# Kernel tuning notes

Measured on AMD Instinct MI355X. Metric: run time of the kernel, lower is better.

## Reference

```python
import jax, jax.numpy as jnp
import numpy as np
from jax import lax

B, N, D, H, K = 4096, 25, 256, 8, 3  # batch*frames, nodes, d_model, heads, conv kernel


def _layernorm(x, g, b, eps=1e-5):
    mu = jnp.mean(x, axis=-1, keepdims=True)
    var = jnp.var(x, axis=-1, keepdims=True)
    return (x - mu) * lax.rsqrt(var + eps) * g + b


def _conv1d(x_bdn, w):
    # x_bdn: [B, D, N], w: [D_out, D_in, K], padding=K//2 (same as torch Conv1d)
    return lax.conv_general_dilated(x_bdn, w, window_strides=(1,),
                                    padding=[(K // 2, K // 2)],
                                    dimension_numbers=('NCH', 'OIH', 'NCH'))


def setup_inputs() -> dict:
    key = jax.random.key(0)
    ks = jax.random.split(key, 12)
    x = jax.random.normal(ks[0], (B, N, D), dtype=jnp.float32)
    # symmetric adjacency with self-loops (skeleton graph surrogate)
    a = jax.random.bernoulli(ks[1], 0.3, (N, N))
    adj = a | a.T | jnp.eye(N, dtype=bool)
    cs = 1.0 / np.sqrt(D * K)
    wq = jax.random.normal(ks[2], (D, D, K), dtype=jnp.float32) * cs
    wk = jax.random.normal(ks[3], (D, D, K), dtype=jnp.float32) * cs
    wv = jax.random.normal(ks[4], (D, D, K), dtype=jnp.float32) * cs
    gq = jnp.ones((D,), jnp.float32); bq = jnp.zeros((D,), jnp.float32)
    gk = jnp.ones((D,), jnp.float32); bk = jnp.zeros((D,), jnp.float32)
    gv = jnp.ones((D,), jnp.float32); bv = jnp.zeros((D,), jnp.float32)
    rel_table = jax.random.normal(ks[5], (2 * N - 1, H), dtype=jnp.float32) * 0.02
    local_bias = jnp.zeros((H, N, N), jnp.float32)
    wo = jax.random.normal(ks[6], (D, D), dtype=jnp.float32) * (1.0 / np.sqrt(D))
    bo = jnp.zeros((D,), jnp.float32)
    return dict(x=x, adj=adj, wq=wq, wk=wk, wv=wv, gq=gq, bq=bq, gk=gk, bk=bk,
                gv=gv, bv=bv, rel_table=rel_table, local_bias=local_bias, wo=wo, bo=bo)


def reference(x, adj, wq, wk, wv, gq, bq, gk, bk, gv, bv, rel_table, local_bias, wo, bo):
    b, n, d = x.shape
    h = local_bias.shape[0]
    dk = d // h
    xp = x.transpose(0, 2, 1)  # [B, D, N]
    # conv QKV projection over node axis + per-projection LayerNorm + residual
    q = x + _layernorm(_conv1d(xp, wq).transpose(0, 2, 1), gq, bq)
    k = x + _layernorm(_conv1d(xp, wk).transpose(0, 2, 1), gk, bk)
    v = x + _layernorm(_conv1d(xp, wv).transpose(0, 2, 1), gv, bv)
    qh = q.reshape(b, n, h, dk).transpose(0, 2, 1, 3)  # [B, H, N, dk]
    kh = k.reshape(b, n, h, dk).transpose(0, 2, 1, 3)
    vh = v.reshape(b, n, h, dk).transpose(0, 2, 1, 3)
    scores = jnp.einsum('bhnd,bhmd->bhnm', qh, kh) / np.sqrt(dk)
    # relative positional bias over node indices
    coords = jnp.arange(n)
    idx = coords[:, None] - coords[None, :] + n - 1  # [N, N]
    rel = rel_table[idx].transpose(2, 0, 1)  # [H, N, N]
    scores = scores + rel[None] + local_bias[None]
    # adjacency mask (local attention): non-neighbors -> -inf
    scores = jnp.where(adj[None, None], scores, jnp.finfo(scores.dtype).min)
    attn = jax.nn.softmax(scores, axis=-1)
    out = jnp.einsum('bhnm,bhmd->bhnd', attn, vh)  # [B, H, N, dk]
    out = out.transpose(0, 2, 1, 3).reshape(b, n, d)
    return out @ wo.T + bo
```

## Files before the change

kernel.cpp:

```cpp
#include <hip/hip_runtime.h>

#define BB 4096
#define NN 25
#define DD 256
#define HH 8
#define DKH 32
#define MM (BB*NN)

typedef __bf16 bf16;
typedef bf16 bf16x8 __attribute__((ext_vector_type(8)));
typedef bf16 bf16x4 __attribute__((ext_vector_type(4)));
typedef float f32x4 __attribute__((ext_vector_type(4)));
typedef _Float16 h16;
typedef h16 h16x2 __attribute__((ext_vector_type(2)));
typedef h16 h16x4 __attribute__((ext_vector_type(4)));
typedef h16 h16x8 __attribute__((ext_vector_type(8)));

__device__ __forceinline__ void async_load16(const void* g, void* l) {
  __builtin_amdgcn_global_load_lds(
      (const __attribute__((address_space(1))) unsigned int*)g,
      (__attribute__((address_space(3))) unsigned int*)l, 16, 0, 0);
}

#define SCHED_FENCE() __builtin_amdgcn_sched_barrier(0)
#define BARRIER() do { SCHED_FENCE(); __builtin_amdgcn_s_barrier(); SCHED_FENCE(); } while (0)

__global__ __launch_bounds__(256) void k_prep_xpad(const float* __restrict__ x,
                                                   bf16* __restrict__ xpad) {
  int idx = (blockIdx.x * 256 + threadIdx.x) * 8;
  const int total = BB * 27 * 256;
  if (idx >= total) return;
  int b = idx / (27 * 256);
  int rem = idx - b * 27 * 256;
  int j = rem >> 8;
  int d = rem & 255;
  bf16x8 o;
  if (j >= 1 && j <= 25) {
    const float* src = x + ((b * 25 + (j - 1)) * 256 + d);
    #pragma unroll
    for (int t = 0; t < 8; ++t) o[t] = (bf16)src[t];
  } else {
    #pragma unroll
    for (int t = 0; t < 8; ++t) o[t] = (bf16)0.0f;
  }
  *(bf16x8*)(xpad + idx) = o;
}

__global__ __launch_bounds__(256) void k_prep_misc(
    const float* __restrict__ wq, const float* __restrict__ wk, const float* __restrict__ wv,
    const float* __restrict__ rel, const float* __restrict__ lb, const float* __restrict__ wo,
    const void* __restrict__ adj_raw,
    bf16* __restrict__ Wt, bf16* __restrict__ woB, float* __restrict__ mb) {
  const int NWT = 768 * 768;
  const int NWO = 256 * 256;
  const int NMB = HH * NN * 32;
  const int total = NWT + NWO + NMB;
  for (int i = blockIdx.x * blockDim.x + threadIdx.x; i < total; i += gridDim.x * blockDim.x) {
    if (i < NWT) {
      int j = i / 768, kk = i - j * 768;
      int proj = j >> 8, jo = j & 255;
      int tap = kk >> 8, di = kk & 255;
      const float* w = (proj == 0) ? wq : ((proj == 1) ? wk : wv);
      Wt[i] = (bf16)w[(jo * 256 + di) * 3 + tap];
    } else if (i < NWT + NWO) {
      int t = i - NWT;
      woB[t] = (bf16)wo[t];
    } else {
      int t = i - NWT - NWO;
      int pair = t >> 5;
      int m = t & 31;
      int h = pair / 25, ii = pair - h * 25;
      float v = -1e30f;
      if (m < 25) {
        const unsigned char* bytes = (const unsigned char*)adj_raw;
        bool u8 = false;
        for (int s = 0; s < 625; ++s) {
          if ((s & 3) && bytes[s]) { u8 = true; break; }
        }
        int amask = u8 ? (bytes[ii * 25 + m] ? 1 : 0)
                       : (((const int*)adj_raw)[ii * 25 + m] ? 1 : 0);
        if (amask)
          v = rel[(ii - m + 24) * HH + h] + lb[h * 625 + ii * 25 + m];
      }
      mb[t] = v;
    }
  }
}

__global__ __launch_bounds__(512, 2) void k_qkv_gemm8(const bf16* __restrict__ xpad,
                                                      const bf16* __restrict__ Wt,
                                                      bf16* __restrict__ conv) {
  __shared__ bf16 Ab[2][256 * 64];
  __shared__ bf16 Bb[2][256 * 64];

  const int L = blockIdx.x;
  const int sw = (L & 7) * 150 + (L >> 3);
  const int n0 = (sw % 3) * 256;
  const int m0 = (sw / 3) * 256;

  const int tid = threadIdx.x;
  const int lane = tid & 63, wave = tid >> 6;
  const int t16 = lane & 15, quad = lane >> 4;
  const int wr = wave >> 2, wc = wave & 3;

  const int srow = tid >> 3;
  const int sc = ((tid & 7) << 4) ^ ((srow & 7) << 4);
  int aOff[4], bOff[4];
  #pragma unroll
  for (int q = 0; q < 4; ++q) {
    int row = q * 64 + srow;
    int gm = m0 + row;
    int b = gm / 25;
    int n = gm - b * 25;
    aOff[q] = (b * 27 + n) * 512 + sc;
    bOff[q] = (n0 + row) * 1536 + sc;
  }

  const int axr = (t16 & 7) << 3;
  int aoffs[2], boffs[2];
  #pragma unroll
  for (int kk = 0; kk < 2; ++kk) {
    aoffs[kk] = (wr * 128 + t16) * 64 + ((kk * 32 + quad * 8) ^ axr);
    boffs[kk] = (wc * 64 + t16) * 64 + ((kk * 32 + quad * 8) ^ axr);
  }

  f32x4 acc[8][4];
  #pragma unroll
  for (int i = 0; i < 8; ++i)
    #pragma unroll
    for (int j = 0; j < 4; ++j) acc[i][j] = (f32x4){0.f, 0.f, 0.f, 0.f};

  #define ST_B(bufi, tt) do {                                              \
    char* lb_ = (char*)&Bb[bufi][0] + wave * 1024;                         \
    _Pragma("unroll")                                                      \
    for (int q_ = 0; q_ < 4; ++q_)                                         \
      async_load16((const char*)Wt + bOff[q_] + (tt) * 128, lb_ + q_ * 8192); \
  } while (0)
  #define ST_A(bufi, tt) do {                                              \
    char* la_ = (char*)&Ab[bufi][0] + wave * 1024;                         \
    const int ka_ = ((tt) >> 2) * 512 + ((tt) & 3) * 128;                  \
    _Pragma("unroll")                                                      \
    for (int q_ = 0; q_ < 4; ++q_)                                         \
      async_load16((const char*)xpad + aOff[q_] + ka_, la_ + q_ * 8192);   \
  } while (0)

  ST_B(0, 0); ST_A(0, 0);
  ST_B(1, 1); ST_A(1, 1);
  asm volatile("s_waitcnt vmcnt(8)" ::: "memory");
  SCHED_FENCE();
  BARRIER();

  bf16x8 aLo[8], aHi[8], bLo[4], bHi[4];
  {
    const bf16* Ac = &Ab[0][0];
    const bf16* Bc = &Bb[0][0];
    #pragma unroll
    for (int i = 0; i < 4; ++i)
      #pragma unroll
      for (int kk = 0; kk < 2; ++kk)
        aLo[i * 2 + kk] = *(const bf16x8*)(Ac + aoffs[kk] + i * 1024);
    #pragma unroll
    for (int j = 0; j < 2; ++j)
      #pragma unroll
      for (int kk = 0; kk < 2; ++kk)
        bLo[j * 2 + kk] = *(const bf16x8*)(Bc + boffs[kk] + j * 1024);
  }
  SCHED_FENCE();

  for (int u = 0; u < 12; ++u) {
    const int buf = u & 1;
    const bf16* Ac = &Ab[buf][0];
    const bf16* Bc = &Bb[buf][0];
    const bf16* Ac2 = &Ab[buf ^ 1][0];
    const bf16* Bc2 = &Bb[buf ^ 1][0];
    const int st = u + 2;

    #pragma unroll
    for (int j = 0; j < 2; ++j)
      #pragma unroll
      for (int kk = 0; kk < 2; ++kk)
        bHi[j * 2 + kk] = *(const bf16x8*)(Bc + boffs[kk] + (2 + j) * 1024);
    SCHED_FENCE();
    __builtin_amdgcn_s_setprio(1);
    #pragma unroll
    for (int i = 0; i < 4; ++i)
      #pragma unroll
      for (int j = 0; j < 2; ++j)
        #pragma unroll
        for (int kk = 0; kk < 2; ++kk)
          acc[i][j] = __builtin_amdgcn_mfma_f32_16x16x32_bf16(
              aLo[i * 2 + kk], bLo[j * 2 + kk], acc[i][j], 0, 0, 0);
    __builtin_amdgcn_s_setprio(0);
    SCHED_FENCE();

    #pragma unroll
    for (int i = 0; i < 4; ++i)
      #pragma unroll
      for (int kk = 0; kk < 2; ++kk)
        aHi[i * 2 + kk] = *(const bf16x8*)(Ac + aoffs[kk] + (4 + i) * 1024);
    SCHED_FENCE();
    __builtin_amdgcn_s_setprio(1);
    #pragma unroll
    for (int i = 0; i < 4; ++i)
      #pragma unroll
      for (int j = 0; j < 2; ++j)
        #pragma unroll
        for (int kk = 0; kk < 2; ++kk)
          acc[i][2 + j] = __builtin_amdgcn_mfma_f32_16x16x32_bf16(
              aLo[i * 2 + kk], bHi[j * 2 + kk], acc[i][2 + j], 0, 0, 0);
    __builtin_amdgcn_s_setprio(0);
    SCHED_FENCE();

    BARRIER();
    if (st < 12) ST_B(buf, st);
    SCHED_FENCE();
    __builtin_amdgcn_s_setprio(1);
    #pragma unroll
    for (int i = 0; i < 4; ++i)
      #pragma unroll
      for (int j = 0; j < 2; ++j)
        #pragma unroll
        for (int kk = 0; kk < 2; ++kk)
          acc[4 + i][j] = __builtin_amdgcn_mfma_f32_16x16x32_bf16(
              aHi[i * 2 + kk], bLo[j * 2 + kk], acc[4 + i][j], 0, 0, 0);
    __builtin_amdgcn_s_setprio(0);
    SCHED_FENCE();

    if (u < 11) {
      if (u < 10) {
        asm volatile("s_waitcnt vmcnt(4)" ::: "memory");
      } else {
        asm volatile("s_waitcnt vmcnt(0)" ::: "memory");
      }
      SCHED_FENCE();
      BARRIER();
      if (st < 12) ST_A(buf, st);
      #pragma unroll
      for (int i = 0; i < 4; ++i)
        #pragma unroll
        for (int kk = 0; kk < 2; ++kk)
          aLo[i * 2 + kk] = *(const bf16x8*)(Ac2 + aoffs[kk] + i * 1024);
      #pragma unroll
      for (int j = 0; j < 2; ++j)
        #pragma unroll
        for (int kk = 0; kk < 2; ++kk)
          bLo[j * 2 + kk] = *(const bf16x8*)(Bc2 + boffs[kk] + j * 1024);
      SCHED_FENCE();
    }
    __builtin_amdgcn_s_setprio(1);
    #pragma unroll
    for (int i = 0; i < 4; ++i)
      #pragma unroll
      for (int j = 0; j < 2; ++j)
        #pragma unroll
        for (int kk = 0; kk < 2; ++kk)
          acc[4 + i][2 + j] = __builtin_amdgcn_mfma_f32_16x16x32_bf16(
              aHi[i * 2 + kk], bHi[j * 2 + kk], acc[4 + i][2 + j], 0, 0, 0);
    __builtin_amdgcn_s_setprio(0);
    SCHED_FENCE();
  }
  #undef ST_A
  #undef ST_B

  #pragma unroll
  for (int i = 0; i < 8; ++i)
    #pragma unroll
    for (int j = 0; j < 4; ++j) {
      const int col = n0 + wc * 64 + j * 16 + t16;
      #pragma unroll
      for (int r = 0; r < 4; ++r) {
        const int rowm = m0 + wr * 128 + i * 16 + quad * 4 + r;
        conv[(size_t)rowm * 768 + col] = (bf16)acc[i][j][r];
      }
    }
}

__global__ __launch_bounds__(256, 4) void k_attn3(
    const bf16* __restrict__ conv, const float* __restrict__ x,
    const float* __restrict__ gq, const float* __restrict__ bq,
    const float* __restrict__ gk, const float* __restrict__ bk,
    const float* __restrict__ gv, const float* __restrict__ bv,
    const float* __restrict__ mb, bf16* __restrict__ attnout) {
  __shared__ bf16 Cs[19456];
  const int b = blockIdx.x;
  const int tid = threadIdx.x;
  const int wave = tid >> 6, lane = tid & 63;

  const char* slab = (const char*)(conv + (size_t)b * 19200);
  for (int c = wave; c < 38; c += 4)
    async_load16(slab + c * 1024 + lane * 16, (char*)Cs + c * 1024);
  asm volatile("s_waitcnt vmcnt(0)" ::: "memory");
  __syncthreads();

  for (int rowi = wave; rowi < 75; rowi += 4) {
    int n = rowi / 3;
    int p = rowi - n * 3;
    const int off = n * 768 + p * 256 + lane * 4;
    bf16x4 cv = *(const bf16x4*)(Cs + off);
    float v0 = (float)cv[0], v1 = (float)cv[1], v2 = (float)cv[2], v3 = (float)cv[3];
    float s = v0 + v1 + v2 + v3;
    float ss = v0 * v0 + v1 * v1 + v2 * v2 + v3 * v3;
    #pragma unroll
    for (int o = 32; o; o >>= 1) {
      s += __shfl_xor(s, o);
      ss += __shfl_xor(ss, o);
    }
    float mu = s * (1.0f / 256.0f);
    float var = ss * (1.0f / 256.0f) - mu * mu;
    float rs = rsqrtf(var + 1e-5f);
    const float* gsel = (p == 0) ? gq : ((p == 1) ? gk : gv);
    const float* bsel = (p == 0) ? bq : ((p == 1) ? bk : bv);
    const int dbase = lane * 4;
    f32x4 gg = *(const f32x4*)(gsel + dbase);
    f32x4 b2 = *(const f32x4*)(bsel + dbase);
    f32x4 xv = *(const f32x4*)(x + ((size_t)(b * 25 + n)) * 256 + dbase);
    h16x4 o;
    o[0] = (h16)((v0 - mu) * rs * gg[0] + b2[0] + xv[0]);
    o[1] = (h16)((v1 - mu) * rs * gg[1] + b2[1] + xv[1]);
    o[2] = (h16)((v2 - mu) * rs * gg[2] + b2[2] + xv[2]);
    o[3] = (h16)((v3 - mu) * rs * gg[3] + b2[3] + xv[3]);
    *(h16x4*)((h16*)Cs + off) = o;
  }
  __syncthreads();

  const h16* Ch = (const h16*)Cs;
  if (tid < HH * NN) {
    const int h = tid / 25;
    const int i = tid - h * 25;

    h16x2 qv[16];
    const h16x2* qp = (const h16x2*)(Ch + i * 768 + h * 32);
    #pragma unroll
    for (int c = 0; c < 16; ++c) qv[c] = qp[c];

    float mrow[28];
    const float* mbp = mb + (h * 25 + i) * 32;
    #pragma unroll
    for (int c = 0; c < 7; ++c) *(f32x4*)(mrow + c * 4) = *(const f32x4*)(mbp + c * 4);

    const float scale = 0.17677669529663687f;
    float sc[25];
    #pragma unroll
    for (int m = 0; m < 25; ++m) {
      const h16x2* kr = (const h16x2*)(Ch + m * 768 + 256 + h * 32);
      float d = 0.f;
      #pragma unroll
      for (int c = 0; c < 16; ++c)
        d = __builtin_amdgcn_fdot2(qv[c], kr[c], d, false);
      sc[m] = d * scale + mrow[m];
    }

    float mx = sc[0];
    #pragma unroll
    for (int m = 1; m < 25; ++m) mx = fmaxf(mx, sc[m]);
    float sum = 0.f;
    #pragma unroll
    for (int m = 0; m < 25; ++m) { sc[m] = __expf(sc[m] - mx); sum += sc[m]; }
    const float inv = 1.0f / sum;

    h16x2 acc[16];
    #pragma unroll
    for (int j = 0; j < 16; ++j) acc[j] = (h16x2){(h16)0.f, (h16)0.f};
    #pragma unroll
    for (int m = 0; m < 25; ++m) {
      h16 w = (h16)(sc[m] * inv);
      h16x2 wp = {w, w};
      const h16x2* vr = (const h16x2*)(Ch + m * 768 + 512 + h * 32);
      #pragma unroll
      for (int j = 0; j < 16; ++j)
        acc[j] = wp * vr[j] + acc[j];
    }

    bf16* dst = attnout + ((size_t)b * 25 + i) * 256 + h * 32;
    #pragma unroll
    for (int c = 0; c < 4; ++c) {
      bf16x8 o;
      #pragma unroll
      for (int j = 0; j < 4; ++j) {
        o[2 * j]     = (bf16)(float)acc[c * 4 + j][0];
        o[2 * j + 1] = (bf16)(float)acc[c * 4 + j][1];
      }
      *(bf16x8*)(dst + c * 8) = o;
    }
  }
}

__global__ __launch_bounds__(256) void k_outproj(const bf16* __restrict__ attn,
                                                 const bf16* __restrict__ woB,
                                                 const float* __restrict__ bo,
                                                 float* __restrict__ out) {
  __shared__ bf16 As[128 * 32];
  __shared__ bf16 Bs[128 * 32];
  const int L = blockIdx.x;
  const int X = L & 7;
  const int t = L >> 3;
  const int n0 = (t & 1) * 128;
  const int m0 = (X + 8 * (t >> 1)) * 128;
  const int tid = threadIdx.x;
  const int wave = tid >> 6, lane = tid & 63;
  const int quad = lane >> 4, t16 = lane & 15;
  const int wr = wave >> 1, wc = wave & 1;

  f32x4 acc[4][4];
  #pragma unroll
  for (int i = 0; i < 4; ++i)
    #pragma unroll
    for (int j = 0; j < 4; ++j) acc[i][j] = (f32x4){0.f, 0.f, 0.f, 0.f};

  const bf16* baseA[2];
  const bf16* baseB[2];
  #pragma unroll
  for (int r = 0; r < 2; ++r) {
    int c = r * 256 + wave * 64 + lane;
    int row = c >> 2, sub = c & 3;
    baseA[r] = attn + (m0 + row) * 256 + sub * 8;
    baseB[r] = woB + (n0 + row) * 256 + sub * 8;
  }

  for (int ks = 0; ks < 256; ks += 32) {
    #pragma unroll
    for (int r = 0; r < 2; ++r)
      async_load16(baseA[r] + ks, As + (r * 256 + wave * 64) * 8);
    #pragma unroll
    for (int r = 0; r < 2; ++r)
      async_load16(baseB[r] + ks, Bs + (r * 256 + wave * 64) * 8);
    asm volatile("s_waitcnt vmcnt(0)" ::: "memory");
    __syncthreads();

    bf16x8 af[4], bfr[4];
    #pragma unroll
    for (int i = 0; i < 4; ++i)
      af[i] = *(const bf16x8*)(As + (wr * 64 + i * 16 + t16) * 32 + quad * 8);
    #pragma unroll
    for (int j = 0; j < 4; ++j)
      bfr[j] = *(const bf16x8*)(Bs + (wc * 64 + j * 16 + t16) * 32 + quad * 8);
    #pragma unroll
    for (int i = 0; i < 4; ++i)
      #pragma unroll
      for (int j = 0; j < 4; ++j)
        acc[i][j] = __builtin_amdgcn_mfma_f32_16x16x32_bf16(af[i], bfr[j], acc[i][j], 0, 0, 0);
    __syncthreads();
  }

  #pragma unroll
  for (int j = 0; j < 4; ++j) {
    int col = n0 + wc * 64 + j * 16 + t16;
    float bb = bo[col];
    #pragma unroll
    for (int i = 0; i < 4; ++i)
      #pragma unroll
      for (int r = 0; r < 4; ++r) {
        int rowm = m0 + wr * 64 + i * 16 + quad * 4 + r;
        out[rowm * 256 + col] = acc[i][j][r] + bb;
      }
  }
}

extern "C" void kernel_launch(void* const* d_in, const int* in_sizes, int n_in,
                              void* d_out, int out_size, void* d_ws, size_t ws_size,
                              hipStream_t stream) {
  (void)in_sizes; (void)n_in; (void)out_size; (void)ws_size;
  const float* x  = (const float*)d_in[0];
  const void*  adj = d_in[1];
  const float* wq = (const float*)d_in[2];
  const float* wk = (const float*)d_in[3];
  const float* wv = (const float*)d_in[4];
  const float* gq = (const float*)d_in[5];
  const float* bq = (const float*)d_in[6];
  const float* gk = (const float*)d_in[7];
  const float* bk = (const float*)d_in[8];
  const float* gv = (const float*)d_in[9];
  const float* bv = (const float*)d_in[10];
  const float* rel = (const float*)d_in[11];
  const float* lb = (const float*)d_in[12];
  const float* wo = (const float*)d_in[13];
  const float* bo = (const float*)d_in[14];
  float* out = (float*)d_out;

  char* ws = (char*)d_ws;
  size_t off = 0;
  auto alloc = [&](size_t bytes) -> void* {
    void* p = ws + off;
    off += (bytes + 255) & ~(size_t)255;
    return p;
  };
  bf16* xpad = (bf16*)alloc((size_t)BB * 27 * 256 * 2);
  bf16* conv = (bf16*)alloc((size_t)MM * 768 * 2);
  bf16* attn = (bf16*)alloc((size_t)MM * 256 * 2);
  bf16* Wt   = (bf16*)alloc((size_t)768 * 768 * 2);
  bf16* woB  = (bf16*)alloc((size_t)256 * 256 * 2);
  float* mb  = (float*)alloc((size_t)HH * NN * 32 * 4);

  hipLaunchKernelGGL(k_prep_xpad, dim3(13824), dim3(256), 0, stream, x, xpad);
  hipLaunchKernelGGL(k_prep_misc, dim3(512), dim3(256), 0, stream,
                     wq, wk, wv, rel, lb, wo, adj, Wt, woB, mb);
  hipLaunchKernelGGL(k_qkv_gemm8, dim3(1200), dim3(512), 0, stream, xpad, Wt, conv);
  hipLaunchKernelGGL(k_attn3, dim3(4096), dim3(256), 0, stream,
                     conv, x, gq, bq, gk, bk, gv, bv, mb, attn);
  hipLaunchKernelGGL(k_outproj, dim3(1600), dim3(256), 0, stream, attn, woB, bo, out);
}
```

Before: 554.9 us.

## Fuse output projection into attention kernel and merge prep kernels

The output projection GEMM is folded into the attention kernel. Each block writes its 25x256 attention output into shared memory as fp16 with an XOR swizzle, then runs 16x16x32 f16 MFMAs against a weight matrix pre-packed into fragment order, adding bias and writing fp32 output directly. This removes the bf16 attention intermediate round trip through global memory and one launch; the two prep kernels are also merged into one launch. The cost is that the 25-row tile pads to 32 rows, so some MFMA work is wasted, and every block re-reads the full wo weights from global or L2.

```diff
diff --git a/kernel.cpp b/kernel.cpp
--- a/kernel.cpp
+++ b/kernel.cpp
@@ -25,48 +25,45 @@
 #define SCHED_FENCE() __builtin_amdgcn_sched_barrier(0)
 #define BARRIER() do { SCHED_FENCE(); __builtin_amdgcn_s_barrier(); SCHED_FENCE(); } while (0)
 
-__global__ __launch_bounds__(256) void k_prep_xpad(const float* __restrict__ x,
-                                                   bf16* __restrict__ xpad) {
-  int idx = (blockIdx.x * 256 + threadIdx.x) * 8;
-  const int total = BB * 27 * 256;
-  if (idx >= total) return;
-  int b = idx / (27 * 256);
-  int rem = idx - b * 27 * 256;
-  int j = rem >> 8;
-  int d = rem & 255;
-  bf16x8 o;
-  if (j >= 1 && j <= 25) {
-    const float* src = x + ((b * 25 + (j - 1)) * 256 + d);
-    #pragma unroll
-    for (int t = 0; t < 8; ++t) o[t] = (bf16)src[t];
-  } else {
-    #pragma unroll
-    for (int t = 0; t < 8; ++t) o[t] = (bf16)0.0f;
-  }
-  *(bf16x8*)(xpad + idx) = o;
-}
-
-__global__ __launch_bounds__(256) void k_prep_misc(
+__global__ __launch_bounds__(256) void k_prep(
+    const float* __restrict__ x, bf16* __restrict__ xpad,
     const float* __restrict__ wq, const float* __restrict__ wk, const float* __restrict__ wv,
     const float* __restrict__ rel, const float* __restrict__ lb, const float* __restrict__ wo,
     const void* __restrict__ adj_raw,
-    bf16* __restrict__ Wt, bf16* __restrict__ woB, float* __restrict__ mb) {
+    bf16* __restrict__ Wt, h16* __restrict__ woF, float* __restrict__ mb) {
+  if (blockIdx.x < 13824) {
+    int idx = (blockIdx.x * 256 + threadIdx.x) * 8;
+    const int total = BB * 27 * 256;
+    if (idx >= total) return;
+    int b = idx / (27 * 256);
+    int rem = idx - b * 27 * 256;
+    int j = rem >> 8;
+    int d = rem & 255;
+    bf16x8 o;
+    if (j >= 1 && j <= 25) {
+      const float* src = x + ((b * 25 + (j - 1)) * 256 + d);
+      #pragma unroll
+      for (int t = 0; t < 8; ++t) o[t] = (bf16)src[t];
+    } else {
+      #pragma unroll
+      for (int t = 0; t < 8; ++t) o[t] = (bf16)0.0f;
+    }
+    *(bf16x8*)(xpad + idx) = o;
+    return;
+  }
   const int NWT = 768 * 768;
-  const int NWO = 256 * 256;
   const int NMB = HH * NN * 32;
-  const int total = NWT + NWO + NMB;
-  for (int i = blockIdx.x * blockDim.x + threadIdx.x; i < total; i += gridDim.x * blockDim.x) {
+  const int NWF = 8 * 16 * 64 * 8;
+  const int total = NWT + NMB + NWF;
+  for (int i = (blockIdx.x - 13824) * 256 + threadIdx.x; i < total; i += 512 * 256) {
     if (i < NWT) {
       int j = i / 768, kk = i - j * 768;
       int proj = j >> 8, jo = j & 255;
       int tap = kk >> 8, di = kk & 255;
       const float* w = (proj == 0) ? wq : ((proj == 1) ? wk : wv);
       Wt[i] = (bf16)w[(jo * 256 + di) * 3 + tap];
-    } else if (i < NWT + NWO) {
+    } else if (i < NWT + NMB) {
       int t = i - NWT;
-      woB[t] = (bf16)wo[t];
-    } else {
-      int t = i - NWT - NWO;
       int pair = t >> 5;
       int m = t & 31;
       int h = pair / 25, ii = pair - h * 25;
@@ -83,6 +80,12 @@
           v = rel[(ii - m + 24) * HH + h] + lb[h * 625 + ii * 25 + m];
       }
       mb[t] = v;
+    } else {
+      int e = i - NWT - NMB;
+      int c = e & 7, ln = (e >> 3) & 63, nt = (e >> 9) & 15, ks = e >> 13;
+      int col = nt * 16 + (ln & 15);
+      int k = ks * 32 + (ln >> 4) * 8 + c;
+      woF[e] = (h16)wo[col * 256 + k];
     }
   }
 }
@@ -275,12 +278,13 @@
     }
 }
 
-__global__ __launch_bounds__(256, 4) void k_attn3(
+__global__ __launch_bounds__(256, 4) void k_attn_oproj(
     const bf16* __restrict__ conv, const float* __restrict__ x,
     const float* __restrict__ gq, const float* __restrict__ bq,
     const float* __restrict__ gk, const float* __restrict__ bk,
     const float* __restrict__ gv, const float* __restrict__ bv,
-    const float* __restrict__ mb, bf16* __restrict__ attnout) {
+    const float* __restrict__ mb, const h16* __restrict__ woF,
+    const float* __restrict__ bo, float* __restrict__ out) {
   __shared__ bf16 Cs[19456];
   const int b = blockIdx.x;
   const int tid = threadIdx.x;
@@ -371,88 +375,57 @@
         acc[j] = wp * vr[j] + acc[j];
     }
 
-    bf16* dst = attnout + ((size_t)b * 25 + i) * 256 + h * 32;
     #pragma unroll
     for (int c = 0; c < 4; ++c) {
-      bf16x8 o;
+      h16x8 o;
       #pragma unroll
       for (int j = 0; j < 4; ++j) {
-        o[2 * j]     = (bf16)(float)acc[c * 4 + j][0];
-        o[2 * j + 1] = (bf16)(float)acc[c * 4 + j][1];
-      }
-      *(bf16x8*)(dst + c * 8) = o;
-    }
-  }
-}
-
-__global__ __launch_bounds__(256) void k_outproj(const bf16* __restrict__ attn,
-                                                 const bf16* __restrict__ woB,
-                                                 const float* __restrict__ bo,
-                                                 float* __restrict__ out) {
-  __shared__ bf16 As[128 * 32];
-  __shared__ bf16 Bs[128 * 32];
-  const int L = blockIdx.x;
-  const int X = L & 7;
-  const int t = L >> 3;
-  const int n0 = (t & 1) * 128;
-  const int m0 = (X + 8 * (t >> 1)) * 128;
-  const int tid = threadIdx.x;
-  const int wave = tid >> 6, lane = tid & 63;
-  const int quad = lane >> 4, t16 = lane & 15;
-  const int wr = wave >> 1, wc = wave & 1;
-
-  f32x4 acc[4][4];
-  #pragma unroll
-  for (int i = 0; i < 4; ++i)
-    #pragma unroll
-    for (int j = 0; j < 4; ++j) acc[i][j] = (f32x4){0.f, 0.f, 0.f, 0.f};
-
-  const bf16* baseA[2];
-  const bf16* baseB[2];
-  #pragma unroll
-  for (int r = 0; r < 2; ++r) {
-    int c = r * 256 + wave * 64 + lane;
-    int row = c >> 2, sub = c & 3;
-    baseA[r] = attn + (m0 + row) * 256 + sub * 8;
-    baseB[r] = woB + (n0 + row) * 256 + sub * 8;
-  }
-
-  for (int ks = 0; ks < 256; ks += 32) {
-    #pragma unroll
-    for (int r = 0; r < 2; ++r)
-      async_load16(baseA[r] + ks, As + (r * 256 + wave * 64) * 8);
-    #pragma unroll
-    for (int r = 0; r < 2; ++r)
-      async_load16(baseB[r] + ks, Bs + (r * 256 + wave * 64) * 8);
-    asm volatile("s_waitcnt vmcnt(0)" ::: "memory");
-    __syncthreads();
-
-    bf16x8 af[4], bfr[4];
-    #pragma unroll
-    for (int i = 0; i < 4; ++i)
-      af[i] = *(const bf16x8*)(As + (wr * 64 + i * 16 + t16) * 32 + quad * 8);
-    #pragma unroll
-    for (int j = 0; j < 4; ++j)
-      bfr[j] = *(const bf16x8*)(Bs + (wc * 64 + j * 16 + t16) * 32 + quad * 8);
-    #pragma unroll
-    for (int i = 0; i < 4; ++i)
-      #pragma unroll
-      for (int j = 0; j < 4; ++j)
-        acc[i][j] = __builtin_amdgcn_mfma_f32_16x16x32_bf16(af[i], bfr[j], acc[i][j], 0, 0, 0);
-    __syncthreads();
-  }
-
-  #pragma unroll
-  for (int j = 0; j < 4; ++j) {
-    int col = n0 + wc * 64 + j * 16 + t16;
-    float bb = bo[col];
-    #pragma unroll
-    for (int i = 0; i < 4; ++i)
-      #pragma unroll
-      for (int r = 0; r < 4; ++r) {
-        int rowm = m0 + wr * 64 + i * 16 + quad * 4 + r;
-        out[rowm * 256 + col] = acc[i][j][r] + bb;
-      }
+        o[2 * j]     = acc[c * 4 + j][0];
+        o[2 * j + 1] = acc[c * 4 + j][1];
+      }
+      const int byteoff = i * 1536 + ((h * 64 + c * 16) ^ ((i & 7) << 4));
+      *(h16x8*)((char*)Cs + byteoff) = o;
+    }
+  }
+  __syncthreads();
+
+  {
+    const int t16 = lane & 15, quad = lane >> 4;
+    f32x4 oacc[2][4];
+    #pragma unroll
+    for (int mt = 0; mt < 2; ++mt)
+      #pragma unroll
+      for (int jj = 0; jj < 4; ++jj) oacc[mt][jj] = (f32x4){0.f, 0.f, 0.f, 0.f};
+    const int arow0 = t16;
+    const int arow1 = (16 + t16 > 24) ? 24 : 16 + t16;
+    #pragma unroll
+    for (int ks = 0; ks < 8; ++ks) {
+      h16x8 aF0, aF1;
+      {
+        const int kb = ks * 64 + quad * 16;
+        aF0 = *(const h16x8*)((const char*)Cs + arow0 * 1536 + (kb ^ ((arow0 & 7) << 4)));
+        aF1 = *(const h16x8*)((const char*)Cs + arow1 * 1536 + (kb ^ ((arow1 & 7) << 4)));
+      }
+      #pragma unroll
+      for (int jj = 0; jj < 4; ++jj) {
+        const h16x8 bF = *(const h16x8*)(woF + ((ks * 16 + wave * 4 + jj) << 9) + lane * 8);
+        oacc[0][jj] = __builtin_amdgcn_mfma_f32_16x16x32_f16(aF0, bF, oacc[0][jj], 0, 0, 0);
+        oacc[1][jj] = __builtin_amdgcn_mfma_f32_16x16x32_f16(aF1, bF, oacc[1][jj], 0, 0, 0);
+      }
+    }
+    #pragma unroll
+    for (int jj = 0; jj < 4; ++jj) {
+      const int col = (wave * 4 + jj) * 16 + t16;
+      const float bb = bo[col];
+      #pragma unroll
+      for (int mt = 0; mt < 2; ++mt)
+        #pragma unroll
+        for (int r = 0; r < 4; ++r) {
+          const int row = mt * 16 + quad * 4 + r;
+          if (row < 25)
+            out[((size_t)b * 25 + row) * 256 + col] = oacc[mt][jj][r] + bb;
+        }
+    }
   }
 }
 
@@ -486,16 +459,13 @@
   };
   bf16* xpad = (bf16*)alloc((size_t)BB * 27 * 256 * 2);
   bf16* conv = (bf16*)alloc((size_t)MM * 768 * 2);
-  bf16* attn = (bf16*)alloc((size_t)MM * 256 * 2);
   bf16* Wt   = (bf16*)alloc((size_t)768 * 768 * 2);
-  bf16* woB  = (bf16*)alloc((size_t)256 * 256 * 2);
+  h16*  woF  = (h16*)alloc((size_t)65536 * 2);
   float* mb  = (float*)alloc((size_t)HH * NN * 32 * 4);
 
-  hipLaunchKernelGGL(k_prep_xpad, dim3(13824), dim3(256), 0, stream, x, xpad);
-  hipLaunchKernelGGL(k_prep_misc, dim3(512), dim3(256), 0, stream,
-                     wq, wk, wv, rel, lb, wo, adj, Wt, woB, mb);
+  hipLaunchKernelGGL(k_prep, dim3(14336), dim3(256), 0, stream,
+                     x, xpad, wq, wk, wv, rel, lb, wo, adj, Wt, woF, mb);
   hipLaunchKernelGGL(k_qkv_gemm8, dim3(1200), dim3(512), 0, stream, xpad, Wt, conv);
-  hipLaunchKernelGGL(k_attn3, dim3(4096), dim3(256), 0, stream,
-                     conv, x, gq, bq, gk, bk, gv, bv, mb, attn);
-  hipLaunchKernelGGL(k_outproj, dim3(1600), dim3(256), 0, stream, attn, woB, bo, out);
+  hipLaunchKernelGGL(k_attn_oproj, dim3(4096), dim3(256), 0, stream,
+                     conv, x, gq, bq, gk, bk, gv, bv, mb, woF, bo, out);
 }
```

Measured after the change: 521.6 us. -6.0%, faster.
